# Performance work log

Hardware: AMD Instinct MI355X
Metric: run time of the kernel (lower is better)

Reference implementation:

```python
import jax, jax.numpy as jnp
import numpy as np

B, C, N, H, S = 2048, 64, 64, 8, 4
D = C // H          # head dim 8
CS = C // S         # per-scale channels 16
CP = C // 4         # pattern memory dim 16


def _conv1d(x, w, b):
    # x: [B, Cin, N], w: [Cout, Cin, 3], 'same' padding
    y = jax.lax.conv_general_dilated(x, w, (1,), ((1, 1),),
                                     dimension_numbers=('NCH', 'OIH', 'NCH'))
    return y + b[None, :, None]


def setup_inputs() -> dict:
    key = jax.random.key(0)
    ks = jax.random.split(key, 20)
    s = 0.05
    f32 = jnp.float32
    return {
        'x': jax.random.normal(ks[0], (B, C, N), f32),
        'points': jax.random.normal(ks[1], (N, 3), f32),
        'conv1_w': jax.random.normal(ks[2], (S, CS, C, 3), f32) * s,
        'conv1_b': jnp.zeros((S, CS), f32),
        'conv2_w': jax.random.normal(ks[3], (S, CS, CS, 3), f32) * s,
        'conv2_b': jnp.zeros((S, CS), f32),
        'pattern_memory': jax.random.normal(ks[4], (64, CP), f32),
        'pm1_w': jax.random.normal(ks[5], (C, C + CP), f32) * s,
        'pm1_b': jnp.zeros((C,), f32),
        'pm2_w': jax.random.normal(ks[6], (C, C), f32) * s,
        'pm2_b': jnp.zeros((C,), f32),
        'q_w': jax.random.normal(ks[7], (C, C), f32) * s,
        'q_b': jnp.zeros((C,), f32),
        'k_w': jax.random.normal(ks[8], (C, C), f32) * s,
        'k_b': jnp.zeros((C,), f32),
        'v_w': jax.random.normal(ks[9], (C, C), f32) * s,
        'v_b': jnp.zeros((C,), f32),
        'in_w': jax.random.normal(ks[10], (3 * C, C), f32) * s,
        'in_b': jnp.zeros((3 * C,), f32),
        'mo_w': jax.random.normal(ks[11], (C, C), f32) * s,
        'mo_b': jnp.zeros((C,), f32),
        'out_w': jax.random.normal(ks[12], (C, C), f32) * s,
        'out_b': jnp.zeros((C,), f32),
        'ln_g': jnp.ones((C,), f32),
        'ln_beta': jnp.zeros((C,), f32),
        'adjacency': jax.random.randint(ks[13], (64, 64), 0, 2, jnp.int32),
    }


def _forward(x, points, conv1_w, conv1_b, conv2_w, conv2_b, pattern_memory,
             pm1_w, pm1_b, pm2_w, pm2_b, q_w, q_b, k_w, k_b, v_w, v_b,
             in_w, in_b, mo_w, mo_b, out_w, out_b, ln_g, ln_beta, adjacency):
    b, c, n = x.shape
    # multi-scale conv stacks (fixed small loop over scales)
    feats = []
    for i in range(S):
        y = jax.nn.relu(_conv1d(x, conv1_w[i], conv1_b[i]))
        y = jax.nn.relu(_conv1d(y, conv2_w[i], conv2_b[i]))
        feats.append(jnp.transpose(y, (0, 2, 1)))  # [B, N, CS]
    combined = jnp.concatenate(feats, axis=-1)     # [B, N, C]
    # pattern memory broadcast per point (N == 64)
    pat = jnp.broadcast_to(pattern_memory[None], (b, n, CP))
    pi = jnp.concatenate([combined, pat], axis=-1)  # [B, N, C+CP]
    pf = jax.nn.relu(pi @ pm1_w.T + pm1_b) @ pm2_w.T + pm2_b  # [B, N, C]
    q = pf @ q_w.T + q_b
    k = pf @ k_w.T + k_b
    v = pf @ v_w.T + v_b
    # nn.MultiheadAttention: internal in_proj + out_proj
    wq, wk, wv = in_w[:C], in_w[C:2 * C], in_w[2 * C:]
    bq, bk, bv = in_b[:C], in_b[C:2 * C], in_b[2 * C:]
    q2 = (q @ wq.T + bq).reshape(b, n, H, D)
    k2 = (k @ wk.T + bk).reshape(b, n, H, D)
    v2 = (v @ wv.T + bv).reshape(b, n, H, D)
    scale = 1.0 / np.sqrt(D).astype(np.float32)
    scores = jnp.einsum('bnhd,bmhd->bhnm', q2, k2) * scale
    attn = jax.nn.softmax(scores, axis=-1)
    ctx = jnp.einsum('bhnm,bmhd->bnhd', attn, v2).reshape(b, n, C)
    attended = ctx @ mo_w.T + mo_b
    # vectorized geometric bias (replaces the 64x64 python loop)
    diff = points[:, None, :] - points[None, :, :]
    dist = jnp.sqrt(jnp.sum(diff * diff, axis=-1) + 1e-12)
    geo = jnp.where(adjacency > 0, jnp.float32(0.5), -0.1 / (1.0 + dist))
    attended = attended + geo[None]
    # layer norm over channels, then output projection
    h = attended + pf
    mu = jnp.mean(h, axis=-1, keepdims=True)
    var = jnp.mean((h - mu) ** 2, axis=-1, keepdims=True)
    hn = (h - mu) * jax.lax.rsqrt(var + 1e-5) * ln_g + ln_beta
    out = hn @ out_w.T + out_b
    return jnp.transpose(out, (0, 2, 1))  # [B, C, N]


def reference(x, points, conv1_w, conv1_b, conv2_w, conv2_b, pattern_memory,
              pm1_w, pm1_b, pm2_w, pm2_b, q_w, q_b, k_w, k_b, v_w, v_b,
              in_w, in_b, mo_w, mo_b, out_w, out_b, ln_g, ln_beta, adjacency):
    return _forward(x, points, conv1_w, conv1_b, conv2_w, conv2_b,
                    pattern_memory, pm1_w, pm1_b, pm2_w, pm2_b, q_w, q_b,
                    k_w, k_b, v_w, v_b, in_w, in_b, mo_w, mo_b, out_w, out_b,
                    ln_g, ln_beta, adjacency)
```

## Files before the change

kernel.cpp:

```cpp
#include <hip/hip_runtime.h>
#include <math.h>

using bf16x8 = __attribute__((ext_vector_type(8))) __bf16;
using f32x4  = __attribute__((ext_vector_type(4))) float;

#if __has_builtin(__builtin_amdgcn_exp2f)
#define EXP2F(x) __builtin_amdgcn_exp2f(x)
#else
#define EXP2F(x) exp2f(x)
#endif

__device__ __forceinline__ unsigned short f2bf(float f) {
  unsigned u = __float_as_uint(f);
  unsigned r = u + 0x7fffu + ((u >> 16) & 1u);
  return (unsigned short)(r >> 16);
}

__device__ __forceinline__ f32x4 mfma16(uint4 a, uint4 b, f32x4 c) {
  return __builtin_amdgcn_mfma_f32_16x16x32_bf16(
      __builtin_bit_cast(bf16x8, a), __builtin_bit_cast(bf16x8, b), c, 0, 0, 0);
}
__device__ __forceinline__ float swz_xor16(float v) {
  return __int_as_float(__builtin_amdgcn_ds_swizzle(__float_as_int(v), 0x401F));
}

#define FRAG_OFF(k, n) (((((n) >> 4) * 2 + ((k) >> 5)) * 64 + (((k) >> 3) & 3) * 16 + ((n) & 15)) * 8 + ((k) & 7))

#define ATT_C 0.51006997f

__global__ void precompute_kernel(
    const float* __restrict__ conv1_w, const float* __restrict__ conv2_w,
    const float* __restrict__ pm1_w, const float* __restrict__ pm1_b,
    const float* __restrict__ pm2_w,
    const float* __restrict__ q_w, const float* __restrict__ q_b,
    const float* __restrict__ k_w, const float* __restrict__ k_b,
    const float* __restrict__ v_w, const float* __restrict__ v_b,
    const float* __restrict__ in_w, const float* __restrict__ in_b,
    const float* __restrict__ mo_w, const float* __restrict__ out_w,
    const float* __restrict__ pattern, const float* __restrict__ points,
    const int* __restrict__ adjacency,
    unsigned short* __restrict__ wsb, float* __restrict__ wsf) {
  int idx = blockIdx.x * 256 + threadIdx.x;
  if (idx < 12288) {
    int t = idx >> 12, rem = idx & 4095;
    int oc = rem >> 6, c = rem & 63;
    wsb[idx] = f2bf(conv1_w[(oc * 64 + c) * 3 + t]);
  } else if (idx < 24576) {
    int i2 = idx - 12288;
    int t = i2 >> 12, rem = i2 & 4095;
    int oc = rem >> 6, ci = rem & 63;
    float v = ((ci >> 4) == (oc >> 4)) ? conv2_w[(oc * 16 + (ci & 15)) * 3 + t] : 0.0f;
    wsb[idx] = f2bf(v);
  } else if (idx < 28672) {
    int rem = idx - 24576;
    wsb[idx] = f2bf(pm1_w[(rem >> 6) * 80 + (rem & 63)]);
  } else if (idx < 32768) {
    wsb[idx] = f2bf(pm2_w[idx - 28672]);
  } else if (idx < 36864) {
    int rem = idx - 32768; int c = rem >> 6, k = rem & 63;
    float s = 0.f;
    #pragma unroll 8
    for (int j = 0; j < 64; ++j) s += in_w[c * 64 + j] * q_w[j * 64 + k];
    wsb[idx] = f2bf(s * ATT_C);
  } else if (idx < 40960) {
    int rem = idx - 36864; int c = rem >> 6, k = rem & 63;
    float s = 0.f;
    #pragma unroll 8
    for (int j = 0; j < 64; ++j) s += in_w[(64 + c) * 64 + j] * k_w[j * 64 + k];
    wsb[idx] = f2bf(s);
  } else if (idx < 45056) {
    int rem = idx - 40960; int c = rem >> 6, k = rem & 63;
    float s = 0.f;
    #pragma unroll 8
    for (int j = 0; j < 64; ++j) s += in_w[(128 + c) * 64 + j] * v_w[j * 64 + k];
    wsb[idx] = f2bf(s);
  } else if (idx < 49152) {
    wsb[idx] = f2bf(mo_w[idx - 45056]);
  } else if (idx < 53248) {
    wsb[idx] = f2bf(out_w[idx - 49152]);
  } else if (idx < 57344) {
    int rem = idx - 53248; int c = rem >> 6, n = rem & 63;
    float s = pm1_b[c];
    #pragma unroll
    for (int cp = 0; cp < 16; ++cp) s += pm1_w[c * 80 + 64 + cp] * pattern[n * 16 + cp];
    wsf[rem] = s;
  } else if (idx < 61440) {
    int rem = idx - 57344; int c = rem >> 6, n = rem & 63;
    float dd = 1e-12f;
    #pragma unroll
    for (int i = 0; i < 3; ++i) { float d = points[n * 3 + i] - points[c * 3 + i]; dd += d * d; }
    float dist = sqrtf(dd);
    wsf[4096 + rem] = (adjacency[n * 64 + c] > 0) ? 0.5f : (-0.1f / (1.0f + dist));
  } else if (idx < 61632) {
    int rem = idx - 61440; int which = rem >> 6, c = rem & 63;
    if (which == 0) {
      float s = in_b[c];
      for (int j = 0; j < 64; ++j) s += in_w[c * 64 + j] * q_b[j];
      wsf[8192 + c] = s * ATT_C;
    } else if (which == 1) {
      float s = in_b[64 + c];
      for (int j = 0; j < 64; ++j) s += in_w[(64 + c) * 64 + j] * k_b[j];
      wsf[8256 + c] = s;
    } else {
      float s = in_b[128 + c];
      for (int j = 0; j < 64; ++j) s += in_w[(128 + c) * 64 + j] * v_b[j];
      wsf[8320 + c] = s;
    }
  }
}

__device__ __forceinline__ void gemm64(const unsigned short* __restrict__ Wg,
                                       const unsigned short* Bf,
                                       int w, int lane, f32x4 acc[4]) {
  const int l15 = lane & 15, lq = lane >> 4;
  #pragma unroll
  for (int s = 0; s < 2; ++s) {
    bf16x8 a = *reinterpret_cast<const bf16x8*>(Wg + (16 * w + l15) * 64 + s * 32 + lq * 8);
    #pragma unroll
    for (int nt = 0; nt < 4; ++nt) {
      bf16x8 bb = *reinterpret_cast<const bf16x8*>(Bf + ((nt * 2 + s) * 64 + lane) * 8);
      acc[nt] = __builtin_amdgcn_mfma_f32_16x16x32_bf16(a, bb, acc[nt], 0, 0, 0);
    }
  }
}

#define SLOT_B 4096
#define KBASE  8704
#define VBASE  13312
#define H32F   2048
#define LNS    6656

__global__ __launch_bounds__(256, 4) void fused_kernel(
    const float* __restrict__ x,
    const unsigned short* __restrict__ wsb, const float* __restrict__ wsf,
    const float* __restrict__ conv1_b, const float* __restrict__ conv2_b,
    const float* __restrict__ pm2_b, const float* __restrict__ mo_b,
    const float* __restrict__ out_b, const float* __restrict__ ln_g,
    const float* __restrict__ ln_beta, float* __restrict__ out) {
  __shared__ __align__(16) unsigned char smem_raw[35840];
  unsigned short* S16 = reinterpret_cast<unsigned short*>(smem_raw);
  float* S32 = reinterpret_cast<float*>(smem_raw);

  const int tid = threadIdx.x;
  const int b = blockIdx.x;
  const int lane = tid & 63;
  const int w = tid >> 6;
  const int l15 = lane & 15;
  const int lq = lane >> 4;
  const int c0 = 16 * w + lq * 4;
  f32x4 pfs[4];

  if (tid < 8) S16[VBASE + tid] = 0;
  {
    const float* xb = x + b * 4096;
    #pragma unroll
    for (int i = 0; i < 4; ++i) {
      int e = (tid + i * 256) * 4;
      int c = e >> 6, n0 = e & 63;
      float4 v = *reinterpret_cast<const float4*>(xb + e);
      S16[FRAG_OFF(c, n0 + 0)] = f2bf(v.x);
      S16[FRAG_OFF(c, n0 + 1)] = f2bf(v.y);
      S16[FRAG_OFF(c, n0 + 2)] = f2bf(v.z);
      S16[FRAG_OFF(c, n0 + 3)] = f2bf(v.w);
    }
  }
  __syncthreads();

  auto conv_pass = [&](const unsigned short* Wg, int srcBase, f32x4 acc[4]) {
    bf16x8 a6[3][2];
    #pragma unroll
    for (int t = 0; t < 3; ++t)
      #pragma unroll
      for (int s = 0; s < 2; ++s)
        a6[t][s] = *reinterpret_cast<const bf16x8*>(Wg + t * 4096 + (16 * w + l15) * 64 + s * 32 + lq * 8);
    #pragma unroll
    for (int nt = 0; nt < 4; ++nt) {
      #pragma unroll
      for (int t = 0; t < 3; ++t) {
        int np = nt * 16 + l15 + (t - 1);
        bool ok = (unsigned)np < 64u;
        int a = srcBase + (((np >> 4) * 2) * 64 + lq * 16 + (np & 15)) * 8;
        int A0 = ok ? a : VBASE;
        int A1 = ok ? (a + 512) : VBASE;
        bf16x8 b0 = *reinterpret_cast<const bf16x8*>(S16 + A0);
        bf16x8 b1 = *reinterpret_cast<const bf16x8*>(S16 + A1);
        acc[nt] = __builtin_amdgcn_mfma_f32_16x16x32_bf16(a6[t][0], b0, acc[nt], 0, 0, 0);
        acc[nt] = __builtin_amdgcn_mfma_f32_16x16x32_bf16(a6[t][1], b1, acc[nt], 0, 0, 0);
      }
    }
  };

  {
    f32x4 acc[4] = {};
    conv_pass(wsb, 0, acc);
    float bia[4] = {conv1_b[c0], conv1_b[c0 + 1], conv1_b[c0 + 2], conv1_b[c0 + 3]};
    #pragma unroll
    for (int nt = 0; nt < 4; ++nt) {
      int n = nt * 16 + l15;
      ushort4 u = make_ushort4(f2bf(fmaxf(acc[nt][0] + bia[0], 0.f)),
                               f2bf(fmaxf(acc[nt][1] + bia[1], 0.f)),
                               f2bf(fmaxf(acc[nt][2] + bia[2], 0.f)),
                               f2bf(fmaxf(acc[nt][3] + bia[3], 0.f)));
      *reinterpret_cast<ushort4*>(S16 + SLOT_B + FRAG_OFF(c0, n)) = u;
    }
  }
  __syncthreads();

  {
    f32x4 acc[4] = {};
    conv_pass(wsb + 12288, SLOT_B, acc);
    float bia[4] = {conv2_b[c0], conv2_b[c0 + 1], conv2_b[c0 + 2], conv2_b[c0 + 3]};
    #pragma unroll
    for (int nt = 0; nt < 4; ++nt) {
      int n = nt * 16 + l15;
      ushort4 u = make_ushort4(f2bf(fmaxf(acc[nt][0] + bia[0], 0.f)),
                               f2bf(fmaxf(acc[nt][1] + bia[1], 0.f)),
                               f2bf(fmaxf(acc[nt][2] + bia[2], 0.f)),
                               f2bf(fmaxf(acc[nt][3] + bia[3], 0.f)));
      *reinterpret_cast<ushort4*>(S16 + FRAG_OFF(c0, n)) = u;
    }
  }
  __syncthreads();

  {
    f32x4 acc[4] = {};
    gemm64(wsb + 24576, S16, w, lane, acc);
    #pragma unroll
    for (int nt = 0; nt < 4; ++nt) {
      int n = nt * 16 + l15;
      ushort4 u = make_ushort4(f2bf(fmaxf(acc[nt][0] + wsf[(c0 + 0) * 64 + n], 0.f)),
                               f2bf(fmaxf(acc[nt][1] + wsf[(c0 + 1) * 64 + n], 0.f)),
                               f2bf(fmaxf(acc[nt][2] + wsf[(c0 + 2) * 64 + n], 0.f)),
                               f2bf(fmaxf(acc[nt][3] + wsf[(c0 + 3) * 64 + n], 0.f)));
      *reinterpret_cast<ushort4*>(S16 + SLOT_B + FRAG_OFF(c0, n)) = u;
    }
  }
  __syncthreads();

  {
    f32x4 acc[4] = {};
    gemm64(wsb + 28672, S16 + SLOT_B, w, lane, acc);
    float bia[4] = {pm2_b[c0], pm2_b[c0 + 1], pm2_b[c0 + 2], pm2_b[c0 + 3]};
    #pragma unroll
    for (int nt = 0; nt < 4; ++nt) {
      int n = nt * 16 + l15;
      f32x4 v;
      #pragma unroll
      for (int r = 0; r < 4; ++r) v[r] = acc[nt][r] + bia[r];
      pfs[nt] = v;
      *reinterpret_cast<ushort4*>(S16 + FRAG_OFF(c0, n)) =
          make_ushort4(f2bf(v[0]), f2bf(v[1]), f2bf(v[2]), f2bf(v[3]));
    }
  }
  __syncthreads();

  {
    f32x4 acc[4] = {};
    gemm64(wsb + 32768, S16, w, lane, acc);
    #pragma unroll
    for (int nt = 0; nt < 4; ++nt) {
      int n = nt * 16 + l15;
      *reinterpret_cast<ushort4*>(S16 + SLOT_B + n * 72 + c0) =
          make_ushort4(f2bf(acc[nt][0] + wsf[8192 + c0]),
                       f2bf(acc[nt][1] + wsf[8192 + c0 + 1]),
                       f2bf(acc[nt][2] + wsf[8192 + c0 + 2]),
                       f2bf(acc[nt][3] + wsf[8192 + c0 + 3]));
    }
  }
  {
    f32x4 acc[4] = {};
    gemm64(wsb + 36864, S16, w, lane, acc);
    #pragma unroll
    for (int nt = 0; nt < 4; ++nt) {
      int n = nt * 16 + l15;
      *reinterpret_cast<ushort4*>(S16 + KBASE + n * 72 + c0) =
          make_ushort4(f2bf(acc[nt][0] + wsf[8256 + c0]),
                       f2bf(acc[nt][1] + wsf[8256 + c0 + 1]),
                       f2bf(acc[nt][2] + wsf[8256 + c0 + 2]),
                       f2bf(acc[nt][3] + wsf[8256 + c0 + 3]));
    }
  }
  {
    f32x4 acc[4] = {};
    gemm64(wsb + 40960, S16, w, lane, acc);
    #pragma unroll
    for (int nt = 0; nt < 4; ++nt) {
      int n = nt * 16 + l15;
      #pragma unroll
      for (int r = 0; r < 4; ++r)
        S16[VBASE + (c0 + r) * 72 + n] = f2bf(acc[nt][r] + wsf[8320 + c0 + r]);
    }
  }
  __syncthreads();

  {
    uint4 vb[2][2];
    #pragma unroll
    for (int rr = 0; rr < 2; ++rr) {
      int h = w + rr * 4;
      #pragma unroll
      for (int ks = 0; ks < 2; ++ks)
        vb[rr][ks] = *reinterpret_cast<const uint4*>(
            S16 + VBASE + (h * 8 + (l15 & 7)) * 72 + ks * 32 + lq * 8);
    }
    __syncthreads();

    const int Pb = VBASE + w * 1152;
    const bool lq0 = (lq == 0);
    #pragma unroll
    for (int rr = 0; rr < 2; ++rr) {
      const int h = w + rr * 4;
      uint4 ka[4];
      #pragma unroll
      for (int mt = 0; mt < 4; ++mt) {
        uint4 t = *reinterpret_cast<const uint4*>(S16 + KBASE + (mt * 16 + l15) * 72 + h * 8);
        ka[mt].x = lq0 ? t.x : 0u; ka[mt].y = lq0 ? t.y : 0u;
        ka[mt].z = lq0 ? t.z : 0u; ka[mt].w = lq0 ? t.w : 0u;
      }
      #pragma unroll
      for (int q = 0; q < 4; ++q) {
        uint4 qb = *reinterpret_cast<const uint4*>(S16 + SLOT_B + (q * 16 + l15) * 72 + h * 8);
        qb.x = lq0 ? qb.x : 0u; qb.y = lq0 ? qb.y : 0u;
        qb.z = lq0 ? qb.z : 0u; qb.w = lq0 ? qb.w : 0u;
        f32x4 sc[4];
        #pragma unroll
        for (int mt = 0; mt < 4; ++mt) {
          f32x4 z = {0.f, 0.f, 0.f, 0.f};
          sc[mt] = mfma16(ka[mt], qb, z);
        }
        float sum = 0.f;
        #pragma unroll
        for (int mt = 0; mt < 4; ++mt)
          #pragma unroll
          for (int r = 0; r < 4; ++r) {
            float e = EXP2F(sc[mt][r]);
            sc[mt][r] = e; sum += e;
          }
        sum += swz_xor16(sum);
        sum += __shfl_xor(sum, 32);
        float inv = __builtin_amdgcn_rcpf(sum);
        #pragma unroll
        for (int mt = 0; mt < 4; ++mt) {
          unsigned d0 = __builtin_amdgcn_perm(__float_as_uint(sc[mt][1] * inv),
                                              __float_as_uint(sc[mt][0] * inv), 0x07060302u);
          unsigned d1 = __builtin_amdgcn_perm(__float_as_uint(sc[mt][3] * inv),
                                              __float_as_uint(sc[mt][2] * inv), 0x07060302u);
          *reinterpret_cast<uint2*>(S16 + Pb + l15 * 72 + mt * 16 + lq * 4) = make_uint2(d0, d1);
        }
        f32x4 ctx = {0.f, 0.f, 0.f, 0.f};
        #pragma unroll
        for (int ks = 0; ks < 2; ++ks) {
          uint4 pa = *reinterpret_cast<const uint4*>(S16 + Pb + l15 * 72 + ks * 32 + lq * 8);
          ctx = mfma16(pa, vb[rr][ks], ctx);
        }
        if (l15 < 8) {
          const int kk = h * 8 + l15;
          #pragma unroll
          for (int r = 0; r < 4; ++r)
            S16[FRAG_OFF(kk, q * 16 + lq * 4 + r)] = f2bf(ctx[r]);
        }
      }
    }
  }
  __syncthreads();

  {
    f32x4 acc[4] = {};
    gemm64(wsb + 45056, S16, w, lane, acc);
    #pragma unroll
    for (int nt = 0; nt < 4; ++nt) {
      int n = nt * 16 + l15;
      #pragma unroll
      for (int r = 0; r < 4; ++r) {
        int c = c0 + r;
        S32[H32F + c * 65 + n] = acc[nt][r] + mo_b[c] + wsf[4096 + c * 64 + n] + pfs[nt][r];
      }
    }
  }
  __syncthreads();

  {
    int n = tid & 63, qq = tid >> 6;
    float sum = 0.f, ssq = 0.f;
    #pragma unroll
    for (int j = 0; j < 16; ++j) {
      float v = S32[H32F + (qq * 16 + j) * 65 + n];
      sum += v; ssq += v * v;
    }
    S32[LNS + tid] = sum;
    S32[LNS + 256 + tid] = ssq;
    __syncthreads();
    if (tid < 64) {
      float s = S32[LNS + tid] + S32[LNS + 64 + tid] + S32[LNS + 128 + tid] + S32[LNS + 192 + tid];
      float ss = S32[LNS + 256 + tid] + S32[LNS + 320 + tid] + S32[LNS + 384 + tid] + S32[LNS + 448 + tid];
      float mu = s * (1.0f / 64.0f);
      float var = ss * (1.0f / 64.0f) - mu * mu;
      S32[LNS + 512 + tid] = mu;
      S32[LNS + 576 + tid] = rsqrtf(var + 1e-5f);
    }
    __syncthreads();
    float mu = S32[LNS + 512 + n], rs = S32[LNS + 576 + n];
    #pragma unroll
    for (int half = 0; half < 2; ++half) {
      int ch0 = qq * 16 + half * 8;
      unsigned short us[8];
      #pragma unroll
      for (int jj = 0; jj < 8; ++jj) {
        int c = ch0 + jj;
        float v = (S32[H32F + c * 65 + n] - mu) * rs * ln_g[c] + ln_beta[c];
        us[jj] = f2bf(v);
      }
      ushort4* p = reinterpret_cast<ushort4*>(S16 + FRAG_OFF(ch0, n));
      p[0] = make_ushort4(us[0], us[1], us[2], us[3]);
      p[1] = make_ushort4(us[4], us[5], us[6], us[7]);
    }
  }
  __syncthreads();

  {
    f32x4 acc[4] = {};
    gemm64(wsb + 49152, S16, w, lane, acc);
    float* ob = out + b * 4096;
    float bia[4] = {out_b[c0], out_b[c0 + 1], out_b[c0 + 2], out_b[c0 + 3]};
    #pragma unroll
    for (int nt = 0; nt < 4; ++nt) {
      int n = nt * 16 + l15;
      #pragma unroll
      for (int r = 0; r < 4; ++r)
        ob[(c0 + r) * 64 + n] = acc[nt][r] + bia[r];
    }
  }
}

extern "C" void kernel_launch(void* const* d_in, const int* in_sizes, int n_in,
                              void* d_out, int out_size, void* d_ws, size_t ws_size,
                              hipStream_t stream) {
  const float* x        = (const float*)d_in[0];
  const float* points   = (const float*)d_in[1];
  const float* conv1_w  = (const float*)d_in[2];
  const float* conv1_b  = (const float*)d_in[3];
  const float* conv2_w  = (const float*)d_in[4];
  const float* conv2_b  = (const float*)d_in[5];
  const float* pattern  = (const float*)d_in[6];
  const float* pm1_w    = (const float*)d_in[7];
  const float* pm1_b    = (const float*)d_in[8];
  const float* pm2_w    = (const float*)d_in[9];
  const float* pm2_b    = (const float*)d_in[10];
  const float* q_w      = (const float*)d_in[11];
  const float* q_b      = (const float*)d_in[12];
  const float* k_w      = (const float*)d_in[13];
  const float* k_b      = (const float*)d_in[14];
  const float* v_w      = (const float*)d_in[15];
  const float* v_b      = (const float*)d_in[16];
  const float* in_w     = (const float*)d_in[17];
  const float* in_b     = (const float*)d_in[18];
  const float* mo_w     = (const float*)d_in[19];
  const float* mo_b     = (const float*)d_in[20];
  const float* out_w    = (const float*)d_in[21];
  const float* out_b    = (const float*)d_in[22];
  const float* ln_g     = (const float*)d_in[23];
  const float* ln_beta  = (const float*)d_in[24];
  const int*   adjacency= (const int*)d_in[25];

  unsigned short* wsb = (unsigned short*)d_ws;
  float* wsf = (float*)((char*)d_ws + 106496);

  precompute_kernel<<<241, 256, 0, stream>>>(
      conv1_w, conv2_w, pm1_w, pm1_b, pm2_w, q_w, q_b, k_w, k_b, v_w, v_b,
      in_w, in_b, mo_w, out_w, pattern, points, adjacency, wsb, wsf);

  fused_kernel<<<2048, 256, 0, stream>>>(
      x, wsb, wsf, conv1_b, conv2_b, pm2_b, mo_b, out_b, ln_g, ln_beta,
      (float*)d_out);
}
```

Baseline: 173.8 us.

## Split work by positions per wave to drop block barriers

Restructures the fused kernel so each wave owns 16 sequence positions across all 64 channels, rather than 16 channels across all positions. Pointwise GEMMs, the QKV projection, per-query attention and the layer norm can then run wave-locally, reading from per-wave LDS scratch. This removes most __syncthreads and the LDS round-trip used for the layer-norm reductions, which now use cross-lane swizzles. Packed bf16 conversions and a transposed precompute layout for the pattern and geometry tables are added to make the loads vectorised. In exchange, each wave loads the full 64x64 weight matrices from global memory for every GEMM (four times the weight traffic), and each wave now does all eight heads for its queries.

```diff
diff --git a/kernel.cpp b/kernel.cpp
--- a/kernel.cpp
+++ b/kernel.cpp
@@ -2,6 +2,7 @@
 #include <math.h>
 
 using bf16x8 = __attribute__((ext_vector_type(8))) __bf16;
+using bf16x2 = __attribute__((ext_vector_type(2))) __bf16;
 using f32x4  = __attribute__((ext_vector_type(4))) float;
 
 #if __has_builtin(__builtin_amdgcn_exp2f)
@@ -15,6 +16,14 @@
   unsigned r = u + 0x7fffu + ((u >> 16) & 1u);
   return (unsigned short)(r >> 16);
 }
+__device__ __forceinline__ unsigned pk_bf16(float lo, float hi) {
+#if __has_builtin(__builtin_amdgcn_cvt_pk_bf16_f32)
+  bf16x2 p = __builtin_amdgcn_cvt_pk_bf16_f32(lo, hi);
+  return __builtin_bit_cast(unsigned, p);
+#else
+  return (unsigned)f2bf(lo) | ((unsigned)f2bf(hi) << 16);
+#endif
+}
 
 __device__ __forceinline__ f32x4 mfma16(uint4 a, uint4 b, f32x4 c) {
   return __builtin_amdgcn_mfma_f32_16x16x32_bf16(
@@ -25,6 +34,7 @@
 }
 
 #define FRAG_OFF(k, n) (((((n) >> 4) * 2 + ((k) >> 5)) * 64 + (((k) >> 3) & 3) * 16 + ((n) & 15)) * 8 + ((k) & 7))
+#define LFRAG_OFF(k, nl) (((((k) >> 5) * 64) + ((((k) >> 3) & 3) * 16) + (nl)) * 8 + ((k) & 7))
 
 #define ATT_C 0.51006997f
 
@@ -83,14 +93,14 @@
     float s = pm1_b[c];
     #pragma unroll
     for (int cp = 0; cp < 16; ++cp) s += pm1_w[c * 80 + 64 + cp] * pattern[n * 16 + cp];
-    wsf[rem] = s;
+    wsf[n * 64 + c] = s;
   } else if (idx < 61440) {
     int rem = idx - 57344; int c = rem >> 6, n = rem & 63;
     float dd = 1e-12f;
     #pragma unroll
     for (int i = 0; i < 3; ++i) { float d = points[n * 3 + i] - points[c * 3 + i]; dd += d * d; }
     float dist = sqrtf(dd);
-    wsf[4096 + rem] = (adjacency[n * 64 + c] > 0) ? 0.5f : (-0.1f / (1.0f + dist));
+    wsf[4096 + n * 64 + c] = (adjacency[n * 64 + c] > 0) ? 0.5f : (-0.1f / (1.0f + dist));
   } else if (idx < 61632) {
     int rem = idx - 61440; int which = rem >> 6, c = rem & 63;
     if (which == 0) {
@@ -109,26 +119,13 @@
   }
 }
 
-__device__ __forceinline__ void gemm64(const unsigned short* __restrict__ Wg,
-                                       const unsigned short* Bf,
-                                       int w, int lane, f32x4 acc[4]) {
-  const int l15 = lane & 15, lq = lane >> 4;
-  #pragma unroll
-  for (int s = 0; s < 2; ++s) {
-    bf16x8 a = *reinterpret_cast<const bf16x8*>(Wg + (16 * w + l15) * 64 + s * 32 + lq * 8);
-    #pragma unroll
-    for (int nt = 0; nt < 4; ++nt) {
-      bf16x8 bb = *reinterpret_cast<const bf16x8*>(Bf + ((nt * 2 + s) * 64 + lane) * 8);
-      acc[nt] = __builtin_amdgcn_mfma_f32_16x16x32_bf16(a, bb, acc[nt], 0, 0, 0);
-    }
-  }
-}
-
-#define SLOT_B 4096
-#define KBASE  8704
-#define VBASE  13312
-#define H32F   2048
-#define LNS    6656
+#define PWSZ   2304
+#define B1OFF  1152
+#define XFB    9216
+#define KB     9216
+#define GUARD  13312
+#define Y1B    13824
+#define VB     13824
 
 __global__ __launch_bounds__(256, 4) void fused_kernel(
     const float* __restrict__ x,
@@ -137,20 +134,52 @@
     const float* __restrict__ pm2_b, const float* __restrict__ mo_b,
     const float* __restrict__ out_b, const float* __restrict__ ln_g,
     const float* __restrict__ ln_beta, float* __restrict__ out) {
-  __shared__ __align__(16) unsigned char smem_raw[35840];
+  __shared__ __align__(16) unsigned char smem_raw[36864];
   unsigned short* S16 = reinterpret_cast<unsigned short*>(smem_raw);
-  float* S32 = reinterpret_cast<float*>(smem_raw);
-
-  const int tid = threadIdx.x;
-  const int b = blockIdx.x;
+
+  const int tid  = threadIdx.x;
+  const int b    = blockIdx.x;
   const int lane = tid & 63;
-  const int w = tid >> 6;
-  const int l15 = lane & 15;
-  const int lq = lane >> 4;
-  const int c0 = 16 * w + lq * 4;
+  const int w    = tid >> 6;
+  const int l15  = lane & 15;
+  const int lq   = lane >> 4;
+  const bool lq0 = (lq == 0);
+  const int ng   = 16 * w + l15;
+  const int PW0  = w * PWSZ;
+  const int PW1  = w * PWSZ + B1OFF;
   f32x4 pfs[4];
 
-  if (tid < 8) S16[VBASE + tid] = 0;
+  auto gemm_cs = [&](const unsigned short* __restrict__ Wg, uint4 b0, uint4 b1,
+                     f32x4 acc[4]) {
+    #pragma unroll
+    for (int ct = 0; ct < 4; ++ct) {
+      uint4 a0 = *reinterpret_cast<const uint4*>(Wg + (ct * 16 + l15) * 64 + lq * 8);
+      uint4 a1 = *reinterpret_cast<const uint4*>(Wg + (ct * 16 + l15) * 64 + 32 + lq * 8);
+      acc[ct] = mfma16(a0, b0, acc[ct]);
+      acc[ct] = mfma16(a1, b1, acc[ct]);
+    }
+  };
+  auto conv_cs = [&](const unsigned short* __restrict__ Wg, int srcBase, f32x4 acc[4]) {
+    #pragma unroll
+    for (int t = 0; t < 3; ++t) {
+      int np = ng + (t - 1);
+      bool ok = (unsigned)np < 64u;
+      int base = srcBase + ((((np >> 4) * 2) * 64) + lq * 16 + (np & 15)) * 8;
+      int A0 = ok ? base : GUARD;
+      int A1 = ok ? (base + 512) : GUARD;
+      uint4 b0 = *reinterpret_cast<const uint4*>(S16 + A0);
+      uint4 b1 = *reinterpret_cast<const uint4*>(S16 + A1);
+      #pragma unroll
+      for (int ct = 0; ct < 4; ++ct) {
+        uint4 a0 = *reinterpret_cast<const uint4*>(Wg + t * 4096 + (ct * 16 + l15) * 64 + lq * 8);
+        uint4 a1 = *reinterpret_cast<const uint4*>(Wg + t * 4096 + (ct * 16 + l15) * 64 + 32 + lq * 8);
+        acc[ct] = mfma16(a0, b0, acc[ct]);
+        acc[ct] = mfma16(a1, b1, acc[ct]);
+      }
+    }
+  };
+
+  if (tid < 8) S16[GUARD + tid] = 0;
   {
     const float* xb = x + b * 4096;
     #pragma unroll
@@ -158,276 +187,230 @@
       int e = (tid + i * 256) * 4;
       int c = e >> 6, n0 = e & 63;
       float4 v = *reinterpret_cast<const float4*>(xb + e);
-      S16[FRAG_OFF(c, n0 + 0)] = f2bf(v.x);
-      S16[FRAG_OFF(c, n0 + 1)] = f2bf(v.y);
-      S16[FRAG_OFF(c, n0 + 2)] = f2bf(v.z);
-      S16[FRAG_OFF(c, n0 + 3)] = f2bf(v.w);
+      S16[XFB + FRAG_OFF(c, n0 + 0)] = f2bf(v.x);
+      S16[XFB + FRAG_OFF(c, n0 + 1)] = f2bf(v.y);
+      S16[XFB + FRAG_OFF(c, n0 + 2)] = f2bf(v.z);
+      S16[XFB + FRAG_OFF(c, n0 + 3)] = f2bf(v.w);
     }
   }
   __syncthreads();
 
-  auto conv_pass = [&](const unsigned short* Wg, int srcBase, f32x4 acc[4]) {
-    bf16x8 a6[3][2];
-    #pragma unroll
-    for (int t = 0; t < 3; ++t)
-      #pragma unroll
-      for (int s = 0; s < 2; ++s)
-        a6[t][s] = *reinterpret_cast<const bf16x8*>(Wg + t * 4096 + (16 * w + l15) * 64 + s * 32 + lq * 8);
-    #pragma unroll
-    for (int nt = 0; nt < 4; ++nt) {
-      #pragma unroll
-      for (int t = 0; t < 3; ++t) {
-        int np = nt * 16 + l15 + (t - 1);
-        bool ok = (unsigned)np < 64u;
-        int a = srcBase + (((np >> 4) * 2) * 64 + lq * 16 + (np & 15)) * 8;
-        int A0 = ok ? a : VBASE;
-        int A1 = ok ? (a + 512) : VBASE;
-        bf16x8 b0 = *reinterpret_cast<const bf16x8*>(S16 + A0);
-        bf16x8 b1 = *reinterpret_cast<const bf16x8*>(S16 + A1);
-        acc[nt] = __builtin_amdgcn_mfma_f32_16x16x32_bf16(a6[t][0], b0, acc[nt], 0, 0, 0);
-        acc[nt] = __builtin_amdgcn_mfma_f32_16x16x32_bf16(a6[t][1], b1, acc[nt], 0, 0, 0);
-      }
-    }
-  };
-
-  {
-    f32x4 acc[4] = {};
-    conv_pass(wsb, 0, acc);
-    float bia[4] = {conv1_b[c0], conv1_b[c0 + 1], conv1_b[c0 + 2], conv1_b[c0 + 3]};
-    #pragma unroll
-    for (int nt = 0; nt < 4; ++nt) {
-      int n = nt * 16 + l15;
-      ushort4 u = make_ushort4(f2bf(fmaxf(acc[nt][0] + bia[0], 0.f)),
-                               f2bf(fmaxf(acc[nt][1] + bia[1], 0.f)),
-                               f2bf(fmaxf(acc[nt][2] + bia[2], 0.f)),
-                               f2bf(fmaxf(acc[nt][3] + bia[3], 0.f)));
-      *reinterpret_cast<ushort4*>(S16 + SLOT_B + FRAG_OFF(c0, n)) = u;
+  {
+    f32x4 acc[4] = {};
+    conv_cs(wsb, XFB, acc);
+    #pragma unroll
+    for (int ct = 0; ct < 4; ++ct) {
+      int k0 = ct * 16 + lq * 4;
+      float4 bi = *reinterpret_cast<const float4*>(conv1_b + k0);
+      *reinterpret_cast<uint2*>(S16 + Y1B + FRAG_OFF(k0, ng)) =
+          make_uint2(pk_bf16(fmaxf(acc[ct][0] + bi.x, 0.f), fmaxf(acc[ct][1] + bi.y, 0.f)),
+                     pk_bf16(fmaxf(acc[ct][2] + bi.z, 0.f), fmaxf(acc[ct][3] + bi.w, 0.f)));
     }
   }
   __syncthreads();
 
   {
     f32x4 acc[4] = {};
-    conv_pass(wsb + 12288, SLOT_B, acc);
-    float bia[4] = {conv2_b[c0], conv2_b[c0 + 1], conv2_b[c0 + 2], conv2_b[c0 + 3]};
-    #pragma unroll
-    for (int nt = 0; nt < 4; ++nt) {
-      int n = nt * 16 + l15;
-      ushort4 u = make_ushort4(f2bf(fmaxf(acc[nt][0] + bia[0], 0.f)),
-                               f2bf(fmaxf(acc[nt][1] + bia[1], 0.f)),
-                               f2bf(fmaxf(acc[nt][2] + bia[2], 0.f)),
-                               f2bf(fmaxf(acc[nt][3] + bia[3], 0.f)));
-      *reinterpret_cast<ushort4*>(S16 + FRAG_OFF(c0, n)) = u;
+    conv_cs(wsb + 12288, Y1B, acc);
+    #pragma unroll
+    for (int ct = 0; ct < 4; ++ct) {
+      int k0 = ct * 16 + lq * 4;
+      float4 bi = *reinterpret_cast<const float4*>(conv2_b + k0);
+      *reinterpret_cast<uint2*>(S16 + PW0 + LFRAG_OFF(k0, l15)) =
+          make_uint2(pk_bf16(fmaxf(acc[ct][0] + bi.x, 0.f), fmaxf(acc[ct][1] + bi.y, 0.f)),
+                     pk_bf16(fmaxf(acc[ct][2] + bi.z, 0.f), fmaxf(acc[ct][3] + bi.w, 0.f)));
     }
   }
   __syncthreads();
 
   {
-    f32x4 acc[4] = {};
-    gemm64(wsb + 24576, S16, w, lane, acc);
-    #pragma unroll
-    for (int nt = 0; nt < 4; ++nt) {
-      int n = nt * 16 + l15;
-      ushort4 u = make_ushort4(f2bf(fmaxf(acc[nt][0] + wsf[(c0 + 0) * 64 + n], 0.f)),
-                               f2bf(fmaxf(acc[nt][1] + wsf[(c0 + 1) * 64 + n], 0.f)),
-                               f2bf(fmaxf(acc[nt][2] + wsf[(c0 + 2) * 64 + n], 0.f)),
-                               f2bf(fmaxf(acc[nt][3] + wsf[(c0 + 3) * 64 + n], 0.f)));
-      *reinterpret_cast<ushort4*>(S16 + SLOT_B + FRAG_OFF(c0, n)) = u;
+    uint4 b0 = *reinterpret_cast<const uint4*>(S16 + PW0 + lane * 8);
+    uint4 b1 = *reinterpret_cast<const uint4*>(S16 + PW0 + (64 + lane) * 8);
+    f32x4 acc[4] = {};
+    gemm_cs(wsb + 24576, b0, b1, acc);
+    #pragma unroll
+    for (int ct = 0; ct < 4; ++ct) {
+      int k0 = ct * 16 + lq * 4;
+      float4 cp = *reinterpret_cast<const float4*>(wsf + ng * 64 + k0);
+      *reinterpret_cast<uint2*>(S16 + PW1 + LFRAG_OFF(k0, l15)) =
+          make_uint2(pk_bf16(fmaxf(acc[ct][0] + cp.x, 0.f), fmaxf(acc[ct][1] + cp.y, 0.f)),
+                     pk_bf16(fmaxf(acc[ct][2] + cp.z, 0.f), fmaxf(acc[ct][3] + cp.w, 0.f)));
+    }
+  }
+
+  {
+    uint4 b0 = *reinterpret_cast<const uint4*>(S16 + PW1 + lane * 8);
+    uint4 b1 = *reinterpret_cast<const uint4*>(S16 + PW1 + (64 + lane) * 8);
+    f32x4 acc[4] = {};
+    gemm_cs(wsb + 28672, b0, b1, acc);
+    #pragma unroll
+    for (int ct = 0; ct < 4; ++ct) {
+      int k0 = ct * 16 + lq * 4;
+      float4 bi = *reinterpret_cast<const float4*>(pm2_b + k0);
+      f32x4 v;
+      #pragma unroll
+      for (int r = 0; r < 4; ++r) v[r] = acc[ct][r] + (&bi.x)[r];
+      pfs[ct] = v;
+      *reinterpret_cast<uint2*>(S16 + PW0 + LFRAG_OFF(k0, l15)) =
+          make_uint2(pk_bf16(v[0], v[1]), pk_bf16(v[2], v[3]));
+    }
+  }
+
+  uint4 qf[8];
+  {
+    uint4 b0 = *reinterpret_cast<const uint4*>(S16 + PW0 + lane * 8);
+    uint4 b1 = *reinterpret_cast<const uint4*>(S16 + PW0 + (64 + lane) * 8);
+    {
+      f32x4 acc[4] = {};
+      gemm_cs(wsb + 32768, b0, b1, acc);
+      #pragma unroll
+      for (int ct = 0; ct < 4; ++ct) {
+        int k0 = ct * 16 + lq * 4;
+        float4 bi = *reinterpret_cast<const float4*>(wsf + 8192 + k0);
+        *reinterpret_cast<uint2*>(S16 + PW1 + l15 * 72 + k0) =
+            make_uint2(pk_bf16(acc[ct][0] + bi.x, acc[ct][1] + bi.y),
+                       pk_bf16(acc[ct][2] + bi.z, acc[ct][3] + bi.w));
+      }
+    }
+    #pragma unroll
+    for (int h = 0; h < 8; ++h) {
+      uint4 t = *reinterpret_cast<const uint4*>(S16 + PW1 + l15 * 72 + h * 8);
+      qf[h].x = lq0 ? t.x : 0u; qf[h].y = lq0 ? t.y : 0u;
+      qf[h].z = lq0 ? t.z : 0u; qf[h].w = lq0 ? t.w : 0u;
+    }
+    {
+      f32x4 acc[4] = {};
+      gemm_cs(wsb + 36864, b0, b1, acc);
+      #pragma unroll
+      for (int ct = 0; ct < 4; ++ct) {
+        int k0 = ct * 16 + lq * 4;
+        float4 bi = *reinterpret_cast<const float4*>(wsf + 8256 + k0);
+        *reinterpret_cast<uint2*>(S16 + KB + ng * 72 + k0) =
+            make_uint2(pk_bf16(acc[ct][0] + bi.x, acc[ct][1] + bi.y),
+                       pk_bf16(acc[ct][2] + bi.z, acc[ct][3] + bi.w));
+      }
+    }
+    {
+      f32x4 acc[4] = {};
+      gemm_cs(wsb + 40960, b0, b1, acc);
+      #pragma unroll
+      for (int ct = 0; ct < 4; ++ct) {
+        int k0 = ct * 16 + lq * 4;
+        float4 bi = *reinterpret_cast<const float4*>(wsf + 8320 + k0);
+        #pragma unroll
+        for (int r = 0; r < 4; ++r)
+          S16[VB + (k0 + r) * 72 + ng] = f2bf(acc[ct][r] + (&bi.x)[r]);
+      }
     }
   }
   __syncthreads();
 
   {
-    f32x4 acc[4] = {};
-    gemm64(wsb + 28672, S16 + SLOT_B, w, lane, acc);
-    float bia[4] = {pm2_b[c0], pm2_b[c0 + 1], pm2_b[c0 + 2], pm2_b[c0 + 3]};
-    #pragma unroll
-    for (int nt = 0; nt < 4; ++nt) {
-      int n = nt * 16 + l15;
-      f32x4 v;
-      #pragma unroll
-      for (int r = 0; r < 4; ++r) v[r] = acc[nt][r] + bia[r];
-      pfs[nt] = v;
-      *reinterpret_cast<ushort4*>(S16 + FRAG_OFF(c0, n)) =
-          make_ushort4(f2bf(v[0]), f2bf(v[1]), f2bf(v[2]), f2bf(v[3]));
-    }
-  }
-  __syncthreads();
-
-  {
-    f32x4 acc[4] = {};
-    gemm64(wsb + 32768, S16, w, lane, acc);
-    #pragma unroll
-    for (int nt = 0; nt < 4; ++nt) {
-      int n = nt * 16 + l15;
-      *reinterpret_cast<ushort4*>(S16 + SLOT_B + n * 72 + c0) =
-          make_ushort4(f2bf(acc[nt][0] + wsf[8192 + c0]),
-                       f2bf(acc[nt][1] + wsf[8192 + c0 + 1]),
-                       f2bf(acc[nt][2] + wsf[8192 + c0 + 2]),
-                       f2bf(acc[nt][3] + wsf[8192 + c0 + 3]));
-    }
-  }
-  {
-    f32x4 acc[4] = {};
-    gemm64(wsb + 36864, S16, w, lane, acc);
-    #pragma unroll
-    for (int nt = 0; nt < 4; ++nt) {
-      int n = nt * 16 + l15;
-      *reinterpret_cast<ushort4*>(S16 + KBASE + n * 72 + c0) =
-          make_ushort4(f2bf(acc[nt][0] + wsf[8256 + c0]),
-                       f2bf(acc[nt][1] + wsf[8256 + c0 + 1]),
-                       f2bf(acc[nt][2] + wsf[8256 + c0 + 2]),
-                       f2bf(acc[nt][3] + wsf[8256 + c0 + 3]));
-    }
-  }
-  {
-    f32x4 acc[4] = {};
-    gemm64(wsb + 40960, S16, w, lane, acc);
-    #pragma unroll
-    for (int nt = 0; nt < 4; ++nt) {
-      int n = nt * 16 + l15;
-      #pragma unroll
-      for (int r = 0; r < 4; ++r)
-        S16[VBASE + (c0 + r) * 72 + n] = f2bf(acc[nt][r] + wsf[8320 + c0 + r]);
-    }
-  }
-  __syncthreads();
-
-  {
-    uint4 vb[2][2];
-    #pragma unroll
-    for (int rr = 0; rr < 2; ++rr) {
-      int h = w + rr * 4;
-      #pragma unroll
-      for (int ks = 0; ks < 2; ++ks)
-        vb[rr][ks] = *reinterpret_cast<const uint4*>(
-            S16 + VBASE + (h * 8 + (l15 & 7)) * 72 + ks * 32 + lq * 8);
-    }
-    __syncthreads();
-
-    const int Pb = VBASE + w * 1152;
-    const bool lq0 = (lq == 0);
-    #pragma unroll
-    for (int rr = 0; rr < 2; ++rr) {
-      const int h = w + rr * 4;
+    #pragma unroll
+    for (int h = 0; h < 8; ++h) {
       uint4 ka[4];
       #pragma unroll
       for (int mt = 0; mt < 4; ++mt) {
-        uint4 t = *reinterpret_cast<const uint4*>(S16 + KBASE + (mt * 16 + l15) * 72 + h * 8);
+        uint4 t = *reinterpret_cast<const uint4*>(S16 + KB + (mt * 16 + l15) * 72 + h * 8);
         ka[mt].x = lq0 ? t.x : 0u; ka[mt].y = lq0 ? t.y : 0u;
         ka[mt].z = lq0 ? t.z : 0u; ka[mt].w = lq0 ? t.w : 0u;
       }
-      #pragma unroll
-      for (int q = 0; q < 4; ++q) {
-        uint4 qb = *reinterpret_cast<const uint4*>(S16 + SLOT_B + (q * 16 + l15) * 72 + h * 8);
-        qb.x = lq0 ? qb.x : 0u; qb.y = lq0 ? qb.y : 0u;
-        qb.z = lq0 ? qb.z : 0u; qb.w = lq0 ? qb.w : 0u;
-        f32x4 sc[4];
+      f32x4 sc[4];
+      #pragma unroll
+      for (int mt = 0; mt < 4; ++mt) {
+        f32x4 z = {0.f, 0.f, 0.f, 0.f};
+        sc[mt] = mfma16(ka[mt], qf[h], z);
+      }
+      float sum = 0.f;
+      #pragma unroll
+      for (int mt = 0; mt < 4; ++mt)
         #pragma unroll
-        for (int mt = 0; mt < 4; ++mt) {
-          f32x4 z = {0.f, 0.f, 0.f, 0.f};
-          sc[mt] = mfma16(ka[mt], qb, z);
+        for (int r = 0; r < 4; ++r) {
+          float e = EXP2F(sc[mt][r]);
+          sc[mt][r] = e; sum += e;
         }
-        float sum = 0.f;
+      sum += swz_xor16(sum);
+      sum += __shfl_xor(sum, 32);
+      float inv = __builtin_amdgcn_rcpf(sum);
+      #pragma unroll
+      for (int mt = 0; mt < 4; ++mt) {
+        unsigned d0 = __builtin_amdgcn_perm(__float_as_uint(sc[mt][1]),
+                                            __float_as_uint(sc[mt][0]), 0x07060302u);
+        unsigned d1 = __builtin_amdgcn_perm(__float_as_uint(sc[mt][3]),
+                                            __float_as_uint(sc[mt][2]), 0x07060302u);
+        *reinterpret_cast<uint2*>(S16 + PW0 + l15 * 72 + mt * 16 + lq * 4) = make_uint2(d0, d1);
+      }
+      f32x4 ctx = {0.f, 0.f, 0.f, 0.f};
+      #pragma unroll
+      for (int ks = 0; ks < 2; ++ks) {
+        uint4 pa = *reinterpret_cast<const uint4*>(S16 + PW0 + l15 * 72 + ks * 32 + lq * 8);
+        uint4 vb = *reinterpret_cast<const uint4*>(S16 + VB + (h * 8 + (l15 & 7)) * 72 + ks * 32 + lq * 8);
+        ctx = mfma16(pa, vb, ctx);
+      }
+      if (l15 < 8) {
+        int chunk = (h >> 2) * 64 + (h & 3) * 16;
         #pragma unroll
-        for (int mt = 0; mt < 4; ++mt)
-          #pragma unroll
-          for (int r = 0; r < 4; ++r) {
-            float e = EXP2F(sc[mt][r]);
-            sc[mt][r] = e; sum += e;
-          }
-        sum += swz_xor16(sum);
-        sum += __shfl_xor(sum, 32);
-        float inv = __builtin_amdgcn_rcpf(sum);
-        #pragma unroll
-        for (int mt = 0; mt < 4; ++mt) {
-          unsigned d0 = __builtin_amdgcn_perm(__float_as_uint(sc[mt][1] * inv),
-                                              __float_as_uint(sc[mt][0] * inv), 0x07060302u);
-          unsigned d1 = __builtin_amdgcn_perm(__float_as_uint(sc[mt][3] * inv),
-                                              __float_as_uint(sc[mt][2] * inv), 0x07060302u);
-          *reinterpret_cast<uint2*>(S16 + Pb + l15 * 72 + mt * 16 + lq * 4) = make_uint2(d0, d1);
-        }
-        f32x4 ctx = {0.f, 0.f, 0.f, 0.f};
-        #pragma unroll
-        for (int ks = 0; ks < 2; ++ks) {
-          uint4 pa = *reinterpret_cast<const uint4*>(S16 + Pb + l15 * 72 + ks * 32 + lq * 8);
-          ctx = mfma16(pa, vb[rr][ks], ctx);
-        }
-        if (l15 < 8) {
-          const int kk = h * 8 + l15;
-          #pragma unroll
-          for (int r = 0; r < 4; ++r)
-            S16[FRAG_OFF(kk, q * 16 + lq * 4 + r)] = f2bf(ctx[r]);
-        }
-      }
-    }
-  }
-  __syncthreads();
-
-  {
-    f32x4 acc[4] = {};
-    gemm64(wsb + 45056, S16, w, lane, acc);
-    #pragma unroll
-    for (int nt = 0; nt < 4; ++nt) {
-      int n = nt * 16 + l15;
-      #pragma unroll
-      for (int r = 0; r < 4; ++r) {
-        int c = c0 + r;
-        S32[H32F + c * 65 + n] = acc[nt][r] + mo_b[c] + wsf[4096 + c * 64 + n] + pfs[nt][r];
-      }
-    }
-  }
-  __syncthreads();
-
-  {
-    int n = tid & 63, qq = tid >> 6;
+        for (int r = 0; r < 4; ++r)
+          S16[PW1 + (chunk + lq * 4 + r) * 8 + l15] = f2bf(ctx[r] * inv);
+      }
+    }
+  }
+
+  f32x4 hv[4];
+  {
+    uint4 b0 = *reinterpret_cast<const uint4*>(S16 + PW1 + lane * 8);
+    uint4 b1 = *reinterpret_cast<const uint4*>(S16 + PW1 + (64 + lane) * 8);
+    f32x4 acc[4] = {};
+    gemm_cs(wsb + 45056, b0, b1, acc);
+    #pragma unroll
+    for (int ct = 0; ct < 4; ++ct) {
+      int k0 = ct * 16 + lq * 4;
+      float4 mb = *reinterpret_cast<const float4*>(mo_b + k0);
+      float4 ge = *reinterpret_cast<const float4*>(wsf + 4096 + ng * 64 + k0);
+      #pragma unroll
+      for (int r = 0; r < 4; ++r)
+        hv[ct][r] = acc[ct][r] + (&mb.x)[r] + (&ge.x)[r] + pfs[ct][r];
+    }
+  }
+
+  {
     float sum = 0.f, ssq = 0.f;
     #pragma unroll
-    for (int j = 0; j < 16; ++j) {
-      float v = S32[H32F + (qq * 16 + j) * 65 + n];
-      sum += v; ssq += v * v;
-    }
-    S32[LNS + tid] = sum;
-    S32[LNS + 256 + tid] = ssq;
-    __syncthreads();
-    if (tid < 64) {
-      float s = S32[LNS + tid] + S32[LNS + 64 + tid] + S32[LNS + 128 + tid] + S32[LNS + 192 + tid];
-      float ss = S32[LNS + 256 + tid] + S32[LNS + 320 + tid] + S32[LNS + 384 + tid] + S32[LNS + 448 + tid];
-      float mu = s * (1.0f / 64.0f);
-      float var = ss * (1.0f / 64.0f) - mu * mu;
-      S32[LNS + 512 + tid] = mu;
-      S32[LNS + 576 + tid] = rsqrtf(var + 1e-5f);
-    }
-    __syncthreads();
-    float mu = S32[LNS + 512 + n], rs = S32[LNS + 576 + n];
-    #pragma unroll
-    for (int half = 0; half < 2; ++half) {
-      int ch0 = qq * 16 + half * 8;
-      unsigned short us[8];
-      #pragma unroll
-      for (int jj = 0; jj < 8; ++jj) {
-        int c = ch0 + jj;
-        float v = (S32[H32F + c * 65 + n] - mu) * rs * ln_g[c] + ln_beta[c];
-        us[jj] = f2bf(v);
-      }
-      ushort4* p = reinterpret_cast<ushort4*>(S16 + FRAG_OFF(ch0, n));
-      p[0] = make_ushort4(us[0], us[1], us[2], us[3]);
-      p[1] = make_ushort4(us[4], us[5], us[6], us[7]);
-    }
-  }
-  __syncthreads();
-
-  {
-    f32x4 acc[4] = {};
-    gemm64(wsb + 49152, S16, w, lane, acc);
+    for (int ct = 0; ct < 4; ++ct)
+      #pragma unroll
+      for (int r = 0; r < 4; ++r) { float v = hv[ct][r]; sum += v; ssq += v * v; }
+    sum += swz_xor16(sum); sum += __shfl_xor(sum, 32);
+    ssq += swz_xor16(ssq); ssq += __shfl_xor(ssq, 32);
+    float mu = sum * (1.0f / 64.0f);
+    float var = ssq * (1.0f / 64.0f) - mu * mu;
+    float rs = rsqrtf(var + 1e-5f);
+    #pragma unroll
+    for (int ct = 0; ct < 4; ++ct) {
+      int k0 = ct * 16 + lq * 4;
+      float4 g4 = *reinterpret_cast<const float4*>(ln_g + k0);
+      float4 b4 = *reinterpret_cast<const float4*>(ln_beta + k0);
+      float h0 = (hv[ct][0] - mu) * rs * g4.x + b4.x;
+      float h1 = (hv[ct][1] - mu) * rs * g4.y + b4.y;
+      float h2 = (hv[ct][2] - mu) * rs * g4.z + b4.z;
+      float h3 = (hv[ct][3] - mu) * rs * g4.w + b4.w;
+      *reinterpret_cast<uint2*>(S16 + PW0 + LFRAG_OFF(k0, l15)) =
+          make_uint2(pk_bf16(h0, h1), pk_bf16(h2, h3));
+    }
+  }
+
+  {
+    uint4 b0 = *reinterpret_cast<const uint4*>(S16 + PW0 + lane * 8);
+    uint4 b1 = *reinterpret_cast<const uint4*>(S16 + PW0 + (64 + lane) * 8);
+    f32x4 acc[4] = {};
+    gemm_cs(wsb + 49152, b0, b1, acc);
     float* ob = out + b * 4096;
-    float bia[4] = {out_b[c0], out_b[c0 + 1], out_b[c0 + 2], out_b[c0 + 3]};
-    #pragma unroll
-    for (int nt = 0; nt < 4; ++nt) {
-      int n = nt * 16 + l15;
+    #pragma unroll
+    for (int ct = 0; ct < 4; ++ct) {
+      int k0 = ct * 16 + lq * 4;
+      float4 bi = *reinterpret_cast<const float4*>(out_b + k0);
       #pragma unroll
       for (int r = 0; r < 4; ++r)
-        ob[(c0 + r) * 64 + n] = acc[nt][r] + bia[r];
+        ob[(k0 + r) * 64 + ng] = acc[ct][r] + (&bi.x)[r];
     }
   }
 }
```

Result: slower. 243.7 us (+40.2%).
